# Kernel tuning notes

Hardware: AMD Instinct MI355X
Metric: run time of the kernel (lower is better)

## Reference

```python
import jax, jax.numpy as jnp
from jax import lax
import numpy as np

KSIZE = 3      # matching patch size
RATE = 2       # down/up-sampling rate
STRIDE = 1
FUSE_K = 3     # diagonal fuse kernel (identity eye(3))
SCALE = 10.0   # softmax_scale


def same_pad(H, k, s):
    out = -(-H // s)
    pt = max((out - 1) * s + k - H, 0)
    return (pt // 2, pt - pt // 2)


def extract_patches(x, k, s):
    # x: [C,H,W] -> patches [L, C, k, k] with TF 'SAME' padding (matches torch extract_image_patches)
    C, H, W = x.shape
    ph = same_pad(H, k, s)
    pw = same_pad(W, k, s)
    xp = jnp.pad(x, ((0, 0), ph, pw))
    Hp, Wp = xp.shape[1], xp.shape[2]
    Ho = (Hp - k) // s + 1
    Wo = (Wp - k) // s + 1
    sl = [xp[:, i:i + (Ho - 1) * s + 1:s, j:j + (Wo - 1) * s + 1:s]
          for i in range(k) for j in range(k)]
    p = jnp.stack(sl, axis=1).reshape(C, k, k, Ho * Wo)  # [C,k,k,L]
    return p.transpose(3, 0, 1, 2)  # [L,C,k,k]


def diag_sum(t, k=FUSE_K):
    # conv2d with eye(k) kernel, SAME padding: out[p,q] = sum_d t[p+d-k//2, q+d-k//2]
    p0 = (k - 1) // 2
    p1 = k - 1 - p0
    tp = jnp.pad(t, ((p0, p1), (p0, p1)))
    H, W = t.shape
    return sum(tp[d:d + H, d:d + W] for d in range(k))


def attend_one(fi, bi):
    # fi, bi: [C,H,W] full resolution
    C, H, W = fi.shape
    kernel = 2 * RATE
    # patches for reconstruction, from full-res background
    raw_w = extract_patches(bi, kernel, RATE * STRIDE)  # [L,C,4,4]
    # nearest downsample by rate for matching
    fs = fi[:, ::RATE, ::RATE]
    bs = bi[:, ::RATE, ::RATE]
    Hs, Ws = fs.shape[1], fs.shape[2]
    L = Hs * Ws
    # matching patches from downscaled background, l2-normalized
    w = extract_patches(bs, KSIZE, STRIDE)  # [L,C,3,3]
    norm = jnp.sqrt(jnp.sum(w * w, axis=(1, 2, 3), keepdims=True))
    wn = (w / jnp.maximum(norm, 1e-4)).reshape(L, -1)  # [L, C*9]
    # correlation conv == im2col matmul: yi[l, q] = <patch_l(b), patch_q(f)>
    fp = extract_patches(fs, KSIZE, 1).reshape(L, -1)  # [HWf, C*9]
    yi = jnp.einsum('lp,qp->lq', wn, fp)  # [HWb, HWf]
    # fuse: propagate scores along diagonals in both orderings
    t = diag_sum(yi)
    t = t.reshape(Hs, Ws, Hs, Ws).transpose(1, 0, 3, 2).reshape(L, L)
    t = diag_sum(t)
    yi = t.reshape(Ws, Hs, Ws, Hs).transpose(1, 0, 3, 2).reshape(L, Hs, Ws)
    # softmax over background-patch axis
    att = jax.nn.softmax(yi * SCALE, axis=0)  # [L,Hs,Ws]
    # conv_transpose2d(att, raw_w, stride=2, padding=1) / 4  via overlap-add
    contrib = jnp.einsum('lhw,lcij->cijhw', att, raw_w)  # [C,4,4,Hs,Ws]
    buf = jnp.zeros((C, 2 * Hs + 2, 2 * Ws + 2), fi.dtype)
    for i in range(kernel):
        for j in range(kernel):
            buf = buf.at[:, i:i + 2 * Hs:2, j:j + 2 * Ws:2].add(contrib[:, i, j])
    return buf[:, 1:2 * Hs + 1, 1:2 * Ws + 1] / 4.0  # [C,H,W]


def conv3x3_elu(x, w, bias):
    y = lax.conv_general_dilated(x, w, (1, 1), [(1, 1), (1, 1)],
                                 dimension_numbers=('NCHW', 'OIHW', 'NCHW'))
    return jax.nn.elu(y + bias[None, :, None, None])


def setup_inputs() -> dict:
    key = jax.random.key(0)
    k1, k2, k3, k4 = jax.random.split(key, 4)
    B, C, H, W = 4, 128, 128, 128
    f = jax.random.normal(k1, (B, C, H, W), jnp.float32)
    b = jax.random.normal(k2, (B, C, H, W), jnp.float32)
    w1 = jax.random.normal(k3, (C, C, 3, 3), jnp.float32) * 0.02
    b1 = jnp.zeros((C,), jnp.float32)
    w2 = jax.random.normal(k4, (C, C, 3, 3), jnp.float32) * 0.02
    b2 = jnp.zeros((C,), jnp.float32)
    return {'f': f, 'b': b, 'w1': w1, 'b1': b1, 'w2': w2, 'b2': b2}


def reference(f, b, w1, b1, w2, b2):
    y = jax.vmap(attend_one)(f, b)  # [B,C,H,W]
    y = conv3x3_elu(y, w1, b1)
    y = conv3x3_elu(y, w2, b2)
    return y
```

## Files before the change

kernel.cpp:

```cpp
#include <hip/hip_runtime.h>
#include <math.h>

using u16 = unsigned short;
using u32 = unsigned int;
typedef _Float16 f16x8 __attribute__((ext_vector_type(8)));
typedef float    f32x4 __attribute__((ext_vector_type(4)));

union F16U { _Float16 h; u16 u; };
__device__ __forceinline__ u16 f2h(float f) { F16U x; x.h = (_Float16)f; return x.u; }
__device__ __forceinline__ float h2f(u16 v) { F16U x; x.u = v; return (float)x.h; }

__device__ __forceinline__ void gl16(const void* g, void* l) {
  __builtin_amdgcn_global_load_lds((const __attribute__((address_space(1))) void*)g,
                                   (__attribute__((address_space(3))) void*)l, 16, 0, 0);
}


__global__ void k_wperm(const float* __restrict__ w, u16* __restrict__ Wp) {
  int idx = blockIdx.x * 256 + threadIdx.x;
  if (idx < 147456) {
    int co = idx / 1152, r = idx - co * 1152, tap = r >> 7, ci = r & 127;
    Wp[idx] = f2h(w[((size_t)co * 128 + ci) * 9 + tap]);
  }
}

__global__ void k_extract(const float* __restrict__ fi, const float* __restrict__ bi,
                          u16* __restrict__ fh, u16* __restrict__ fl,
                          u16* __restrict__ bh, u16* __restrict__ bl) {
  __shared__ u16 lt[4][64][136];
  int ph = blockIdx.x, t = threadIdx.x;
  for (int it = 0; it < 32; ++it) {
    int idx = it * 256 + t;
    int c = idx >> 6, pw = idx & 63;
    int src = c * 16384 + (2 * ph) * 128 + 2 * pw;
    float vf = fi[src], vb = bi[src];
    u16 fhi = f2h(vf), flo = f2h(vf - h2f(fhi));
    u16 bhi = f2h(vb), blo = f2h(vb - h2f(bhi));
    lt[0][pw][c] = fhi; lt[1][pw][c] = flo; lt[2][pw][c] = bhi; lt[3][pw][c] = blo;
  }
  __syncthreads();
  for (int it = 0; it < 16; ++it) {
    int g = it * 256 + t;
    int arr = g >> 10, rem = g & 1023, pw = rem >> 4, slot = rem & 15;
    uint4 v = *(const uint4*)&lt[arr][pw][slot * 8];
    u16* o = (arr == 0) ? fh : (arr == 1) ? fl : (arr == 2) ? bh : bl;
    *(uint4*)&o[(size_t)(ph * 64 + pw) * 128 + slot * 8] = v;
  }
}

__global__ void k_norm(const u16* __restrict__ bh, const u16* __restrict__ bl,
                       float* __restrict__ nrm) {
  int wid = threadIdx.x >> 6, lane = threadIdx.x & 63;
  int l = blockIdx.x * 4 + wid;
  int lh = l >> 6, lw = l & 63;
  float s = 0.f;
#pragma unroll
  for (int dh = -1; dh <= 1; ++dh)
#pragma unroll
    for (int dw = -1; dw <= 1; ++dw) {
      int y = lh + dh, x = lw + dw;
      if ((u32)y < 64u && (u32)x < 64u) {
        int p = y * 64 + x;
        u32 h2 = *(const u32*)&bh[(size_t)p * 128 + lane * 2];
        u32 l2 = *(const u32*)&bl[(size_t)p * 128 + lane * 2];
        float v0 = h2f((u16)h2) + h2f((u16)l2);
        float v1 = h2f((u16)(h2 >> 16)) + h2f((u16)(l2 >> 16));
        s += v0 * v0 + v1 * v1;
      }
    }
#pragma unroll
  for (int off = 32; off; off >>= 1) s += __shfl_xor(s, off);
  if (lane == 0) nrm[l] = sqrtf(s);
}

__global__ __launch_bounds__(256) void k_rgemm(const u16* __restrict__ fh, const u16* __restrict__ fl,
                                               const u16* __restrict__ bh, const u16* __restrict__ bl,
                                               float* __restrict__ C) {
  __shared__ u16 lds[4 * 128 * 64];
  u16* Ah = lds; u16* Al = lds + 8192; u16* Bh = lds + 16384; u16* Bl = lds + 24576;
  int t = threadIdx.x, lane = t & 63, wid = t >> 6;
  int wm = (wid >> 1) * 64, wn = (wid & 1) * 64;
  int fr = lane & 15, kb = lane >> 4;
  int q0 = blockIdx.y * 128, l0 = blockIdx.x * 128;
  f32x4 acc[4][4] = {};
  for (int kt = 0; kt < 128; kt += 64) {
#pragma unroll
    for (int j = 0; j < 4; ++j) {
      int g = wid * 256 + j * 64 + lane;
      int row = g >> 3, s = (g & 7) ^ (row & 7);
      int co = kt + s * 8;
      size_t ldso = (size_t)(wid * 256 + j * 64) * 8;
      gl16(&fh[(size_t)(q0 + row) * 128 + co], Ah + ldso);
      gl16(&fl[(size_t)(q0 + row) * 128 + co], Al + ldso);
      gl16(&bh[(size_t)(l0 + row) * 128 + co], Bh + ldso);
      gl16(&bl[(size_t)(l0 + row) * 128 + co], Bl + ldso);
    }
    __syncthreads();
#pragma unroll
    for (int kf = 0; kf < 2; ++kf) {
      f16x8 ah[4], al4[4], bh4[4], bl4[4];
#pragma unroll
      for (int mi = 0; mi < 4; ++mi) {
        int row = wm + mi * 16 + fr;
        int off = row * 64 + ((kf * 4 + kb) ^ (row & 7)) * 8;
        ah[mi] = *(const f16x8*)&Ah[off];
        al4[mi] = *(const f16x8*)&Al[off];
      }
#pragma unroll
      for (int ni = 0; ni < 4; ++ni) {
        int row = wn + ni * 16 + fr;
        int off = row * 64 + ((kf * 4 + kb) ^ (row & 7)) * 8;
        bh4[ni] = *(const f16x8*)&Bh[off];
        bl4[ni] = *(const f16x8*)&Bl[off];
      }
#pragma unroll
      for (int mi = 0; mi < 4; ++mi)
#pragma unroll
        for (int ni = 0; ni < 4; ++ni) {
          acc[mi][ni] = __builtin_amdgcn_mfma_f32_16x16x32_f16(ah[mi], bh4[ni], acc[mi][ni], 0, 0, 0);
          acc[mi][ni] = __builtin_amdgcn_mfma_f32_16x16x32_f16(ah[mi], bl4[ni], acc[mi][ni], 0, 0, 0);
          acc[mi][ni] = __builtin_amdgcn_mfma_f32_16x16x32_f16(al4[mi], bh4[ni], acc[mi][ni], 0, 0, 0);
        }
    }
    __syncthreads();
  }
#pragma unroll
  for (int mi = 0; mi < 4; ++mi) {
    int qr = q0 + wm + mi * 16 + kb * 4;
#pragma unroll
    for (int ni = 0; ni < 4; ++ni) {
      int lc = l0 + wn + ni * 16 + fr;
#pragma unroll
      for (int r = 0; r < 4; ++r)
        C[(size_t)(qr + r) * 4096 + lc] = acc[mi][ni][r];
    }
  }
}


__global__ __launch_bounds__(256) void k_passA(const float* __restrict__ R, const float* __restrict__ nrm,
                                               float* __restrict__ Y0) {
  int idx0 = (blockIdx.x * 256 + threadIdx.x) * 4;
  int q = idx0 >> 12, l0 = idx0 & 4095;
  int qh = q >> 6, qw = q & 63, lh = l0 >> 6, lw0 = l0 & 63;
  float a0 = 0.f, a1 = 0.f, a2 = 0.f, a3 = 0.f;
#define TAPA(dh, dw)                                                                   \
  {                                                                                    \
    constexpr int s = (dh) * 64 + (dw);                                                \
    constexpr int r = s & 3;                                                           \
    bool ok = ((u32)(qh + (dh)) < 64u) && ((u32)(qw + (dw)) < 64u) &&                  \
              ((u32)(lh + (dh)) < 64u);                                                \
    int ab = idx0 + s * 4097 - r;                                                      \
    ab = ab < 0 ? 0 : (ab > 16777208 ? 16777208 : ab);                                 \
    float4 lo = *(const float4*)&R[ab], hi = *(const float4*)&R[ab + 4];               \
    float xx[8] = {lo.x, lo.y, lo.z, lo.w, hi.x, hi.y, hi.z, hi.w};                    \
    if (ok) {                                                                          \
      if ((u32)(lw0 + 0 + (dw)) < 64u) a0 += xx[r + 0];                                \
      if ((u32)(lw0 + 1 + (dw)) < 64u) a1 += xx[r + 1];                                \
      if ((u32)(lw0 + 2 + (dw)) < 64u) a2 += xx[r + 2];                                \
      if ((u32)(lw0 + 3 + (dw)) < 64u) a3 += xx[r + 3];                                \
    }                                                                                  \
  }
  TAPA(-1, -1) TAPA(-1, 0) TAPA(-1, 1)
  TAPA(0, -1)  TAPA(0, 0)  TAPA(0, 1)
  TAPA(1, -1)  TAPA(1, 0)  TAPA(1, 1)
#undef TAPA
  float4 nv = *(const float4*)&nrm[l0];
  float4 o;
  o.x = a0 / fmaxf(nv.x, 1e-4f);
  o.y = a1 / fmaxf(nv.y, 1e-4f);
  o.z = a2 / fmaxf(nv.z, 1e-4f);
  o.w = a3 / fmaxf(nv.w, 1e-4f);
  *(float4*)&Y0[idx0] = o;
}

__global__ __launch_bounds__(256) void k_passB(const float* __restrict__ T1, float* __restrict__ Out) {
  int idx0 = (blockIdx.x * 256 + threadIdx.x) * 4;
  int q = idx0 >> 12, l0 = idx0 & 4095;
  int qh = q >> 6, lh = l0 >> 6;
  if (qh >= 2 && qh <= 61 && lh >= 2 && lh <= 61) {
    float a0 = 0.f, a1 = 0.f, a2 = 0.f, a3 = 0.f;
#define TAPB(s_)                                                                       \
  {                                                                                    \
    constexpr int s = (s_);                                                            \
    constexpr int r = s & 3;                                                           \
    const float* p = T1 + (idx0 + s * 4097 - r);                                       \
    float4 lo = *(const float4*)p, hi = *(const float4*)(p + 4);                       \
    float xx[8] = {lo.x, lo.y, lo.z, lo.w, hi.x, hi.y, hi.z, hi.w};                    \
    a0 += xx[r + 0]; a1 += xx[r + 1]; a2 += xx[r + 2]; a3 += xx[r + 3];                \
  }
    TAPB(-65) TAPB(-64) TAPB(-63)
    TAPB(-1)  TAPB(0)   TAPB(1)
    TAPB(63)  TAPB(64)  TAPB(65)
#undef TAPB
    float4 o; o.x = a0; o.y = a1; o.z = a2; o.w = a3;
    *(float4*)&Out[idx0] = o;
  } else {
    float4 o;
    float* oe = (float*)&o;
#pragma unroll
    for (int e = 0; e < 4; ++e) {
      int l = l0 + e;
      int pl = ((l & 63) << 6) | (l >> 6);
      int pq = ((q & 63) << 6) | (q >> 6);
      float acc = 0.f;
#pragma unroll
      for (int e2 = -1; e2 <= 1; ++e2) {
        int pa = pl + e2, pb = pq + e2;
        if ((u32)pa < 4096u && (u32)pb < 4096u) {
          int a = ((pa & 63) << 6) | (pa >> 6);
          int b = ((pb & 63) << 6) | (pb >> 6);
#pragma unroll
          for (int e1 = -1; e1 <= 1; ++e1) {
            int aa = a + e1, bb = b + e1;
            if ((u32)aa < 4096u && (u32)bb < 4096u) acc += T1[(size_t)bb * 4096 + aa];
          }
        }
      }
      oe[e] = acc;
    }
    *(float4*)&Out[idx0] = o;
  }
}

__global__ __launch_bounds__(256) void k_softmax(const float* __restrict__ S, u16* __restrict__ att) {
  int q = blockIdx.x, t = threadIdx.x;
  const float* row = S + (size_t)q * 4096;
  float4 v[4];
  float m = -3.4e38f;
#pragma unroll
  for (int i = 0; i < 4; ++i) {
    v[i] = *(const float4*)&row[i * 1024 + t * 4];
    m = fmaxf(m, fmaxf(fmaxf(v[i].x, v[i].y), fmaxf(v[i].z, v[i].w)));
  }
#pragma unroll
  for (int off = 32; off; off >>= 1) m = fmaxf(m, __shfl_xor(m, off));
  __shared__ float redm[4], reds[4];
  int wid = t >> 6, lane = t & 63;
  if (lane == 0) redm[wid] = m;
  __syncthreads();
  m = fmaxf(fmaxf(redm[0], redm[1]), fmaxf(redm[2], redm[3]));
  float s = 0.f;
#pragma unroll
  for (int i = 0; i < 4; ++i) {
    v[i].x = expf(10.f * (v[i].x - m)); v[i].y = expf(10.f * (v[i].y - m));
    v[i].z = expf(10.f * (v[i].z - m)); v[i].w = expf(10.f * (v[i].w - m));
    s += v[i].x + v[i].y + v[i].z + v[i].w;
  }
#pragma unroll
  for (int off = 32; off; off >>= 1) s += __shfl_xor(s, off);
  if (lane == 0) reds[wid] = s;
  __syncthreads();
  s = reds[0] + reds[1] + reds[2] + reds[3];
  float inv = 1.f / s;
  u16* arow = att + (size_t)q * 4096;
#pragma unroll
  for (int i = 0; i < 4; ++i) {
    union { u16 h[4]; uint2 u; } pk;
    pk.h[0] = f2h(v[i].x * inv); pk.h[1] = f2h(v[i].y * inv);
    pk.h[2] = f2h(v[i].z * inv); pk.h[3] = f2h(v[i].w * inv);
    *(uint2*)&arow[i * 1024 + t * 4] = pk.u;
  }
}

__global__ void k_rwt(const float* __restrict__ bi, u16* __restrict__ RWt) {
  int tid = blockIdx.x * 256 + threadIdx.x;
  int m = tid >> 10, lq = (tid & 1023) * 4;
  int c = m >> 4, i = (m >> 2) & 3, j = m & 3;
  int y = 2 * (lq >> 6) - 1 + i;
  union { u16 h[4]; uint2 u; } pk;
#pragma unroll
  for (int e = 0; e < 4; ++e) {
    int x = 2 * ((lq + e) & 63) - 1 + j;
    float v = 0.f;
    if ((u32)y < 128u && (u32)x < 128u) v = bi[c * 16384 + y * 128 + x];
    pk.h[e] = f2h(v);
  }
  *(uint2*)&RWt[(size_t)m * 4096 + lq] = pk.u;
}

__global__ __launch_bounds__(256) void k_gemm_pv(const u16* __restrict__ A, const u16* __restrict__ Bt,
                                                 float* __restrict__ C) {
  __shared__ u16 lds[2 * 128 * 64];
  u16* la = lds; u16* lb = lds + 8192;
  int t = threadIdx.x, lane = t & 63, wid = t >> 6;
  int wm = (wid >> 1) * 64, wn = (wid & 1) * 64;
  int fr = lane & 15, kb = lane >> 4;
  int m0 = blockIdx.y * 128, n0 = blockIdx.x * 128;
  f32x4 acc[4][4] = {};
  for (int kt = 0; kt < 4096; kt += 64) {
#pragma unroll
    for (int j = 0; j < 4; ++j) {
      int g = wid * 256 + j * 64 + lane;
      int row = g >> 3, s = (g & 7) ^ (row & 7);
      size_t ldso = (size_t)(wid * 256 + j * 64) * 8;
      gl16(&A[(size_t)(m0 + row) * 4096 + kt + s * 8], la + ldso);
      gl16(&Bt[(size_t)(n0 + row) * 4096 + kt + s * 8], lb + ldso);
    }
    __syncthreads();
#pragma unroll
    for (int ks = 0; ks < 2; ++ks) {
      f16x8 af[4], bfr[4];
#pragma unroll
      for (int mi = 0; mi < 4; ++mi) {
        int row = wm + mi * 16 + fr;
        af[mi] = *(const f16x8*)&la[row * 64 + ((ks * 32 + kb * 8) ^ ((row & 7) << 3))];
      }
#pragma unroll
      for (int ni = 0; ni < 4; ++ni) {
        int row = wn + ni * 16 + fr;
        bfr[ni] = *(const f16x8*)&lb[row * 64 + ((ks * 32 + kb * 8) ^ ((row & 7) << 3))];
      }
#pragma unroll
      for (int mi = 0; mi < 4; ++mi)
#pragma unroll
        for (int ni = 0; ni < 4; ++ni)
          acc[mi][ni] = __builtin_amdgcn_mfma_f32_16x16x32_f16(af[mi], bfr[ni], acc[mi][ni], 0, 0, 0);
    }
    __syncthreads();
  }
#pragma unroll
  for (int mi = 0; mi < 4; ++mi) {
    int mr = m0 + wm + mi * 16 + kb * 4;
#pragma unroll
    for (int ni = 0; ni < 4; ++ni) {
      int nc = n0 + wn + ni * 16 + fr;
#pragma unroll
      for (int r = 0; r < 4; ++r)
        C[(size_t)(mr + r) * 2048 + nc] = acc[mi][ni][r];
    }
  }
}

__global__ void k_overlap(const float* __restrict__ O, u16* __restrict__ Yh) {
  int idx = blockIdx.x * 256 + threadIdx.x;
  int c = idx & 127, pix = idx >> 7;
  int ox = pix & 127, oy = pix >> 7;
  int py = oy + 1, px = ox + 1;
  float s = 0.f;
#pragma unroll
  for (int di = 0; di < 2; ++di) {
    int i = (py & 1) + 2 * di;
    int hs = (py - i) >> 1;
    if ((u32)hs >= 64u) continue;
#pragma unroll
    for (int dj = 0; dj < 2; ++dj) {
      int j = (px & 1) + 2 * dj;
      int wsx = (px - j) >> 1;
      if ((u32)wsx >= 64u) continue;
      s += O[(size_t)(hs * 64 + wsx) * 2048 + c * 16 + i * 4 + j];
    }
  }
  Yh[idx] = f2h(0.25f * s);
}

template<int OUT_F16>
__global__ __launch_bounds__(256) void k_conv(const u16* __restrict__ In, const u16* __restrict__ Wp,
                                              const float* __restrict__ bias, void* __restrict__ out_,
                                              const u16* __restrict__ zg) {
  __shared__ u16 lds[2 * 128 * 64];
  u16* la = lds; u16* lb = lds + 8192;
  int t = threadIdx.x, lane = t & 63, wid = t >> 6;
  int wm = (wid >> 1) * 64, wn = (wid & 1) * 64;
  int fr = lane & 15, kb = lane >> 4;
  int yrow = blockIdx.x, bidx = blockIdx.y;
  const u16* inH = In + (size_t)bidx * 2097152;
  f32x4 acc[4][4] = {};
  for (int step = 0; step < 18; ++step) {
    int tap = step >> 1, ci0 = (step & 1) * 64;
    int dy = tap / 3, dx = tap - 3 * (tap / 3);
    int y = yrow + dy - 1;
#pragma unroll
    for (int j = 0; j < 4; ++j) {
      int g = wid * 256 + j * 64 + lane;
      int row = g >> 3, s = (g & 7) ^ (row & 7);
      size_t ldso = (size_t)(wid * 256 + j * 64) * 8;
      gl16(&Wp[(size_t)row * 1152 + step * 64 + s * 8], la + ldso);
      int xx = row + dx - 1;
      const u16* src = ((u32)y < 128u && (u32)xx < 128u)
                         ? &inH[((size_t)y * 128 + xx) * 128 + ci0 + s * 8] : zg;
      gl16(src, lb + ldso);
    }
    __syncthreads();
#pragma unroll
    for (int ks = 0; ks < 2; ++ks) {
      f16x8 af[4], bfr[4];
#pragma unroll
      for (int mi = 0; mi < 4; ++mi) {
        int row = wm + mi * 16 + fr;
        af[mi] = *(const f16x8*)&la[row * 64 + ((ks * 32 + kb * 8) ^ ((row & 7) << 3))];
      }
#pragma unroll
      for (int ni = 0; ni < 4; ++ni) {
        int row = wn + ni * 16 + fr;
        bfr[ni] = *(const f16x8*)&lb[row * 64 + ((ks * 32 + kb * 8) ^ ((row & 7) << 3))];
      }
#pragma unroll
      for (int mi = 0; mi < 4; ++mi)
#pragma unroll
        for (int ni = 0; ni < 4; ++ni)
          acc[mi][ni] = __builtin_amdgcn_mfma_f32_16x16x32_f16(af[mi], bfr[ni], acc[mi][ni], 0, 0, 0);
    }
    __syncthreads();
  }
#pragma unroll
  for (int mi = 0; mi < 4; ++mi) {
    int co = wm + mi * 16 + kb * 4;
#pragma unroll
    for (int ni = 0; ni < 4; ++ni) {
      int x = wn + ni * 16 + fr;
      if (OUT_F16) {
        union { u16 h[4]; uint2 v; } pk;
#pragma unroll
        for (int r = 0; r < 4; ++r) {
          float val = acc[mi][ni][r] + bias[co + r];
          val = val > 0.f ? val : expm1f(val);
          pk.h[r] = f2h(val);
        }
        u16* oH = (u16*)out_ + (size_t)bidx * 2097152;
        *(uint2*)&oH[((size_t)yrow * 128 + x) * 128 + co] = pk.v;
      } else {
        float* oF = (float*)out_ + (size_t)bidx * 2097152;
#pragma unroll
        for (int r = 0; r < 4; ++r) {
          float val = acc[mi][ni][r] + bias[co + r];
          val = val > 0.f ? val : expm1f(val);
          oF[(size_t)(co + r) * 16384 + yrow * 128 + x] = val;
        }
      }
    }
  }
}


extern "C" void kernel_launch(void* const* d_in, const int* in_sizes, int n_in,
                              void* d_out, int out_size, void* d_ws, size_t ws_size,
                              hipStream_t stream) {
  const float* f  = (const float*)d_in[0];
  const float* b  = (const float*)d_in[1];
  const float* w1 = (const float*)d_in[2];
  const float* b1 = (const float*)d_in[3];
  const float* w2 = (const float*)d_in[4];
  const float* b2 = (const float*)d_in[5];
  float* out = (float*)d_out;
  char* ws = (char*)d_ws;

  float* S0   = (float*)(ws);
  float* S1   = (float*)(ws + 67108864);
  u16*   fsTh = (u16*)(ws + 134217728);
  u16*   fsTl = (u16*)(ws + 135266304);
  u16*   bsTh = (u16*)(ws + 136314880);
  u16*   bsTl = (u16*)(ws + 137363456);
  float* nrm  = (float*)(ws + 138412032);
  u16*   Yh   = (u16*)(ws + 138428416);
  u16*   Wp1  = (u16*)(ws + 155205632);
  u16*   Wp2  = (u16*)(ws + 155500544);
  u16*   att  = (u16*)S1;
  u16*   RWt  = (u16*)S0;
  float* O    = (float*)(ws + 16777216);
  u16*   Z1h  = (u16*)S0;
  u16*   zg   = (u16*)(ws + 50331648);

  k_wperm<<<576, 256, 0, stream>>>(w1, Wp1);
  k_wperm<<<576, 256, 0, stream>>>(w2, Wp2);

  for (int i = 0; i < 4; ++i) {
    const float* fb = f + (size_t)i * 2097152;
    const float* bb = b + (size_t)i * 2097152;
    k_extract<<<64, 256, 0, stream>>>(fb, bb, fsTh, fsTl, bsTh, bsTl);
    k_norm<<<1024, 256, 0, stream>>>(bsTh, bsTl, nrm);
    k_rgemm<<<dim3(32, 32), 256, 0, stream>>>(fsTh, fsTl, bsTh, bsTl, S0);
    k_passA<<<16384, 256, 0, stream>>>(S0, nrm, S1);
    k_passB<<<16384, 256, 0, stream>>>(S1, S0);
    k_softmax<<<4096, 256, 0, stream>>>(S0, att);
    k_rwt<<<8192, 256, 0, stream>>>(bb, RWt);
    k_gemm_pv<<<dim3(16, 32), 256, 0, stream>>>(att, RWt, O);
    k_overlap<<<8192, 256, 0, stream>>>(O, Yh + (size_t)i * 2097152);
  }

  hipMemsetAsync(zg, 0, 256, stream);
  k_conv<1><<<dim3(128, 4), 256, 0, stream>>>(Yh, Wp1, b1, Z1h, zg);
  k_conv<0><<<dim3(128, 4), 256, 0, stream>>>(Z1h, Wp2, b2, out, zg);

  (void)in_sizes; (void)n_in; (void)out_size; (void)ws_size;
}
```

Before: 1.218 ms.

## Fuse second diagonal pass into softmax, double-buffer PV GEMM with swizzled grid

Merges the second diagonal-sum pass into the softmax kernel. Each block now computes its 4096-element score row directly from the first-pass output instead of writing it to a float buffer and reading it back, which removes a 64MB round trip per image. The PV GEMM gains LDS double buffering, so the next K tile's global-to-LDS loads overlap the current tile's MFMAs. It also gets a 1D grid with remapped block indices for better L2 locality. Buffers are reassigned so that att, RWt and O no longer overlap; the cost is doubled LDS in the GEMM and more work per thread in the fused kernel.

```diff
diff --git a/kernel.cpp b/kernel.cpp
--- a/kernel.cpp
+++ b/kernel.cpp
@@ -136,7 +136,6 @@
     }
   }
 }
-
 
 __global__ __launch_bounds__(256) void k_passA(const float* __restrict__ R, const float* __restrict__ nrm,
                                                float* __restrict__ Y0) {
@@ -174,65 +173,61 @@
   *(float4*)&Y0[idx0] = o;
 }
 
-__global__ __launch_bounds__(256) void k_passB(const float* __restrict__ T1, float* __restrict__ Out) {
-  int idx0 = (blockIdx.x * 256 + threadIdx.x) * 4;
-  int q = idx0 >> 12, l0 = idx0 & 4095;
-  int qh = q >> 6, lh = l0 >> 6;
-  if (qh >= 2 && qh <= 61 && lh >= 2 && lh <= 61) {
+__global__ __launch_bounds__(256) void k_pbsm(const float* __restrict__ T1, u16* __restrict__ att) {
+  int q = blockIdx.x, t = threadIdx.x;
+  int qh = q >> 6;
+  bool qok = (qh >= 2 && qh <= 61);
+  float v[16];
+#pragma unroll
+  for (int p = 0; p < 4; ++p) {
+    int l0 = p * 1024 + t * 4;
+    int idx0 = q * 4096 + l0;
+    int lh = l0 >> 6;
     float a0 = 0.f, a1 = 0.f, a2 = 0.f, a3 = 0.f;
+    if (qok && lh >= 2 && lh <= 61) {
 #define TAPB(s_)                                                                       \
   {                                                                                    \
     constexpr int s = (s_);                                                            \
     constexpr int r = s & 3;                                                           \
-    const float* p = T1 + (idx0 + s * 4097 - r);                                       \
-    float4 lo = *(const float4*)p, hi = *(const float4*)(p + 4);                       \
+    const float* pp = T1 + (idx0 + s * 4097 - r);                                      \
+    float4 lo = *(const float4*)pp, hi = *(const float4*)(pp + 4);                     \
     float xx[8] = {lo.x, lo.y, lo.z, lo.w, hi.x, hi.y, hi.z, hi.w};                    \
     a0 += xx[r + 0]; a1 += xx[r + 1]; a2 += xx[r + 2]; a3 += xx[r + 3];                \
   }
-    TAPB(-65) TAPB(-64) TAPB(-63)
-    TAPB(-1)  TAPB(0)   TAPB(1)
-    TAPB(63)  TAPB(64)  TAPB(65)
+      TAPB(-65) TAPB(-64) TAPB(-63)
+      TAPB(-1)  TAPB(0)   TAPB(1)
+      TAPB(63)  TAPB(64)  TAPB(65)
 #undef TAPB
-    float4 o; o.x = a0; o.y = a1; o.z = a2; o.w = a3;
-    *(float4*)&Out[idx0] = o;
-  } else {
-    float4 o;
-    float* oe = (float*)&o;
-#pragma unroll
-    for (int e = 0; e < 4; ++e) {
-      int l = l0 + e;
-      int pl = ((l & 63) << 6) | (l >> 6);
-      int pq = ((q & 63) << 6) | (q >> 6);
-      float acc = 0.f;
-#pragma unroll
-      for (int e2 = -1; e2 <= 1; ++e2) {
-        int pa = pl + e2, pb = pq + e2;
-        if ((u32)pa < 4096u && (u32)pb < 4096u) {
-          int a = ((pa & 63) << 6) | (pa >> 6);
-          int b = ((pb & 63) << 6) | (pb >> 6);
-#pragma unroll
-          for (int e1 = -1; e1 <= 1; ++e1) {
-            int aa = a + e1, bb = b + e1;
-            if ((u32)aa < 4096u && (u32)bb < 4096u) acc += T1[(size_t)bb * 4096 + aa];
+    } else {
+      float oe[4];
+#pragma unroll
+      for (int e = 0; e < 4; ++e) {
+        int l = l0 + e;
+        int pl = ((l & 63) << 6) | (l >> 6);
+        int pq = ((q & 63) << 6) | (q >> 6);
+        float acc = 0.f;
+#pragma unroll
+        for (int e2 = -1; e2 <= 1; ++e2) {
+          int pa = pl + e2, pb = pq + e2;
+          if ((u32)pa < 4096u && (u32)pb < 4096u) {
+            int a = ((pa & 63) << 6) | (pa >> 6);
+            int bq = ((pb & 63) << 6) | (pb >> 6);
+#pragma unroll
+            for (int e1 = -1; e1 <= 1; ++e1) {
+              int aa = a + e1, bb = bq + e1;
+              if ((u32)aa < 4096u && (u32)bb < 4096u) acc += T1[(size_t)bb * 4096 + aa];
+            }
           }
         }
-      }
-      oe[e] = acc;
-    }
-    *(float4*)&Out[idx0] = o;
-  }
-}
-
-__global__ __launch_bounds__(256) void k_softmax(const float* __restrict__ S, u16* __restrict__ att) {
-  int q = blockIdx.x, t = threadIdx.x;
-  const float* row = S + (size_t)q * 4096;
-  float4 v[4];
+        oe[e] = acc;
+      }
+      a0 = oe[0]; a1 = oe[1]; a2 = oe[2]; a3 = oe[3];
+    }
+    v[p * 4 + 0] = a0; v[p * 4 + 1] = a1; v[p * 4 + 2] = a2; v[p * 4 + 3] = a3;
+  }
   float m = -3.4e38f;
 #pragma unroll
-  for (int i = 0; i < 4; ++i) {
-    v[i] = *(const float4*)&row[i * 1024 + t * 4];
-    m = fmaxf(m, fmaxf(fmaxf(v[i].x, v[i].y), fmaxf(v[i].z, v[i].w)));
-  }
+  for (int i = 0; i < 16; ++i) m = fmaxf(m, v[i]);
 #pragma unroll
   for (int off = 32; off; off >>= 1) m = fmaxf(m, __shfl_xor(m, off));
   __shared__ float redm[4], reds[4];
@@ -242,11 +237,7 @@
   m = fmaxf(fmaxf(redm[0], redm[1]), fmaxf(redm[2], redm[3]));
   float s = 0.f;
 #pragma unroll
-  for (int i = 0; i < 4; ++i) {
-    v[i].x = expf(10.f * (v[i].x - m)); v[i].y = expf(10.f * (v[i].y - m));
-    v[i].z = expf(10.f * (v[i].z - m)); v[i].w = expf(10.f * (v[i].w - m));
-    s += v[i].x + v[i].y + v[i].z + v[i].w;
-  }
+  for (int i = 0; i < 16; ++i) { v[i] = expf(10.f * (v[i] - m)); s += v[i]; }
 #pragma unroll
   for (int off = 32; off; off >>= 1) s += __shfl_xor(s, off);
   if (lane == 0) reds[wid] = s;
@@ -255,11 +246,11 @@
   float inv = 1.f / s;
   u16* arow = att + (size_t)q * 4096;
 #pragma unroll
-  for (int i = 0; i < 4; ++i) {
+  for (int p = 0; p < 4; ++p) {
     union { u16 h[4]; uint2 u; } pk;
-    pk.h[0] = f2h(v[i].x * inv); pk.h[1] = f2h(v[i].y * inv);
-    pk.h[2] = f2h(v[i].z * inv); pk.h[3] = f2h(v[i].w * inv);
-    *(uint2*)&arow[i * 1024 + t * 4] = pk.u;
+    pk.h[0] = f2h(v[p * 4 + 0] * inv); pk.h[1] = f2h(v[p * 4 + 1] * inv);
+    pk.h[2] = f2h(v[p * 4 + 2] * inv); pk.h[3] = f2h(v[p * 4 + 3] * inv);
+    *(uint2*)&arow[p * 1024 + t * 4] = pk.u;
   }
 }
 
@@ -281,23 +272,35 @@
 
 __global__ __launch_bounds__(256) void k_gemm_pv(const u16* __restrict__ A, const u16* __restrict__ Bt,
                                                  float* __restrict__ C) {
-  __shared__ u16 lds[2 * 128 * 64];
-  u16* la = lds; u16* lb = lds + 8192;
+  __shared__ u16 lds[2 * 16384];
   int t = threadIdx.x, lane = t & 63, wid = t >> 6;
   int wm = (wid >> 1) * 64, wn = (wid & 1) * 64;
   int fr = lane & 15, kb = lane >> 4;
-  int m0 = blockIdx.y * 128, n0 = blockIdx.x * 128;
+  int bid = blockIdx.x;
+  int my = (bid & 7) * 4 + ((bid >> 3) & 3);
+  int nx = bid >> 5;
+  int m0 = my * 128, n0 = nx * 128;
   f32x4 acc[4][4] = {};
+#define STAGE(buf, kt)                                                                  \
+  {                                                                                     \
+    u16* lA = lds + (buf) * 16384;                                                      \
+    u16* lB = lA + 8192;                                                                \
+    _Pragma("unroll")                                                                   \
+    for (int j = 0; j < 4; ++j) {                                                       \
+      int g = wid * 256 + j * 64 + lane;                                                \
+      int row = g >> 3, sw = (g & 7) ^ (row & 7);                                       \
+      size_t ldso = (size_t)(wid * 256 + j * 64) * 8;                                   \
+      gl16(&A[(size_t)(m0 + row) * 4096 + (kt) + sw * 8], lA + ldso);                   \
+      gl16(&Bt[(size_t)(n0 + row) * 4096 + (kt) + sw * 8], lB + ldso);                  \
+    }                                                                                   \
+  }
+  STAGE(0, 0)
+  __syncthreads();
+  int cur = 0;
   for (int kt = 0; kt < 4096; kt += 64) {
-#pragma unroll
-    for (int j = 0; j < 4; ++j) {
-      int g = wid * 256 + j * 64 + lane;
-      int row = g >> 3, s = (g & 7) ^ (row & 7);
-      size_t ldso = (size_t)(wid * 256 + j * 64) * 8;
-      gl16(&A[(size_t)(m0 + row) * 4096 + kt + s * 8], la + ldso);
-      gl16(&Bt[(size_t)(n0 + row) * 4096 + kt + s * 8], lb + ldso);
-    }
-    __syncthreads();
+    if (kt + 64 < 4096) STAGE(cur ^ 1, kt + 64)
+    u16* la = lds + cur * 16384;
+    u16* lb = la + 8192;
 #pragma unroll
     for (int ks = 0; ks < 2; ++ks) {
       f16x8 af[4], bfr[4];
@@ -318,7 +321,9 @@
           acc[mi][ni] = __builtin_amdgcn_mfma_f32_16x16x32_f16(af[mi], bfr[ni], acc[mi][ni], 0, 0, 0);
     }
     __syncthreads();
-  }
+    cur ^= 1;
+  }
+#undef STAGE
 #pragma unroll
   for (int mi = 0; mi < 4; ++mi) {
     int mr = m0 + wm + mi * 16 + kb * 4;
@@ -455,9 +460,9 @@
   u16*   Yh   = (u16*)(ws + 138428416);
   u16*   Wp1  = (u16*)(ws + 155205632);
   u16*   Wp2  = (u16*)(ws + 155500544);
-  u16*   att  = (u16*)S1;
-  u16*   RWt  = (u16*)S0;
-  float* O    = (float*)(ws + 16777216);
+  u16*   att  = (u16*)S0;
+  u16*   RWt  = (u16*)S1;
+  float* O    = (float*)(ws + 67108864 + 16777216);
   u16*   Z1h  = (u16*)S0;
   u16*   zg   = (u16*)(ws + 50331648);
 
@@ -471,10 +476,9 @@
     k_norm<<<1024, 256, 0, stream>>>(bsTh, bsTl, nrm);
     k_rgemm<<<dim3(32, 32), 256, 0, stream>>>(fsTh, fsTl, bsTh, bsTl, S0);
     k_passA<<<16384, 256, 0, stream>>>(S0, nrm, S1);
-    k_passB<<<16384, 256, 0, stream>>>(S1, S0);
-    k_softmax<<<4096, 256, 0, stream>>>(S0, att);
+    k_pbsm<<<4096, 256, 0, stream>>>(S1, att);
     k_rwt<<<8192, 256, 0, stream>>>(bb, RWt);
-    k_gemm_pv<<<dim3(16, 32), 256, 0, stream>>>(att, RWt, O);
+    k_gemm_pv<<<512, 256, 0, stream>>>(att, RWt, O);
     k_overlap<<<8192, 256, 0, stream>>>(O, Yh + (size_t)i * 2097152);
   }
 
```

New measurement: 1.122 ms. -7.9%, faster.
